# Performance work log

Measured on AMD Instinct MI355X. Metric: run time of the kernel, lower is better.

Reference implementation:

```python
import jax, jax.numpy as jnp
import numpy as np

EPS = 1e-3          # module eps
LAPLACE_EPS = 1e-5  # LaplaceModel eps
N_TAPS = 5
N_DELAY = 1
N_ITER = 5


def _mag_sq(x):
    return x.real ** 2 + x.imag ** 2


def _laplace_weights(Y):
    # LaplaceModel: r = 1 / clamp(2*sqrt(sum_f |Y|^2), eps), broadcast over freq
    denom = 2.0 * jnp.sqrt(jnp.sum(_mag_sq(Y), axis=-2, keepdims=True))
    w = 1.0 / jnp.maximum(denom, LAPLACE_EPS)
    return jnp.broadcast_to(w, Y.shape)


def _make_xbar(X):
    # X_bar[..., c, f, t, n] = X[..., c, f, n - (N_TAPS + N_DELAY) + t], zero-padded
    pad = N_TAPS + N_DELAY
    n_frames = X.shape[-1]
    pad_cfg = [(0, 0)] * (X.ndim - 1) + [(pad, 0)]
    Xp = jnp.pad(X, pad_cfg)
    taps = [Xp[..., t:t + n_frames] for t in range(N_TAPS)]
    return jnp.stack(taps, axis=-2)  # (..., n_chan, n_freq, n_taps, n_frames)


def _demix_derev(X, X_bar, W, H):
    reverb = jnp.einsum('...cfdt,...dftn->...cfn', H, X_bar)
    sep = jnp.einsum('...cfd,...dfn->...cfn', W, X)
    return sep - reverb


def _one_iter(Y, X_bar, W, H):
    n_src = Y.shape[-3]
    n_chan = X_bar.shape[-4]
    n_frames = Y.shape[-1]
    weights = _laplace_weights(Y)
    # rescaling step
    g = jnp.maximum(jnp.mean(_mag_sq(Y), axis=(-2, -1), keepdims=True), EPS)
    gs = jnp.sqrt(g)
    Y = Y / jnp.maximum(gs, EPS)
    W = W / jnp.maximum(gs, EPS)
    H = H / jnp.maximum(gs[..., None], EPS)
    weights = weights * g
    # ISS source updates (type 1)
    inv_nf = 1.0 / n_frames
    for src in range(n_src):
        Ys = Y[..., src, :, :]
        v_num = jnp.einsum('...cfn,...cfn,...fn->...cf', weights, Y, Ys.conj()) * inv_nf
        v_den = jnp.einsum('...cfn,...fn->...cf', weights, _mag_sq(Ys)) * inv_nf
        v = v_num / jnp.maximum(v_den, EPS)
        v_s = 1.0 - 1.0 / jnp.sqrt(jnp.maximum(v_den[..., src, :], EPS))
        v = v.at[..., src, :].set(v_s.astype(v.dtype))
        Y = Y - v[..., None] * Ys[..., None, :, :]
        W = W - jnp.einsum('...cf,...fd->...cfd', v, W[..., src, :, :])
        H = H - jnp.einsum('...cf,...fdt->...cfdt', v, H[..., src, :, :, :])
    # ISS tap updates (type 3)
    for src in range(n_chan):
        for tap in range(N_TAPS):
            Xst = X_bar[..., src, :, tap, :]
            v_num = jnp.einsum('...cfn,...cfn,...fn->...cf', weights, Y, Xst.conj())
            v_den = jnp.einsum('...cfn,...fn->...cf', weights, _mag_sq(Xst))
            v = v_num / jnp.maximum(v_den, EPS)
            Y = Y - v[..., None] * Xst[..., None, :, :]
            H = H.at[..., src, tap].add(v)
    return Y, W, H


def _forward(X):
    batch_shape = X.shape[:-3]
    n_chan, n_freq, n_frames = X.shape[-3:]
    n_src = n_chan  # determined case (n_src=None)
    X_bar = _make_xbar(X)
    eye = jnp.maximum(jnp.eye(n_src, n_chan, dtype=X.real.dtype), EPS)
    W = jnp.broadcast_to(eye[:, None, :].astype(X.dtype), batch_shape + (n_src, n_freq, n_chan))
    H = jnp.zeros(batch_shape + (n_src, n_freq, n_chan, N_TAPS), dtype=X.dtype)
    Y = _demix_derev(X, X_bar, W, H)
    for _ in range(N_ITER):
        Y, W, H = _one_iter(Y, X_bar, W, H)
    return jnp.stack([Y.real, Y.imag], axis=0)


def setup_inputs() -> dict:
    key = jax.random.key(0)
    k1, k2 = jax.random.split(key)
    shape = (2, 4, 512, 1000)  # (batch, n_chan, n_freq, n_frames)
    X_real = jax.random.normal(k1, shape, dtype=jnp.float32)
    X_imag = jax.random.normal(k2, shape, dtype=jnp.float32)
    return {"X_real": X_real, "X_imag": X_imag}


def reference(X_real, X_imag):
    X = jax.lax.complex(X_real, X_imag)
    return _forward(X)
```

## Files before the change

### kernel.cpp

```cpp
#include <hip/hip_runtime.h>


constexpr int NCH = 4;
constexpr int NFQ = 512;
constexpr int NFR = 1000;
constexpr int NIT = 5;
constexpr float EPSV  = 1e-3f;
constexpr float INVNF = 1.0f / 1000.0f;
constexpr float INVFN = 1.0f / (512.0f * 1000.0f);
constexpr size_t PLANE = 4096000;
constexpr size_t CSTRIDE = (size_t)NFQ * NFR;

__device__ __forceinline__ float fast_rcp(float x) { return __builtin_amdgcn_rcpf(x); }
__device__ __forceinline__ float fast_rsq(float x) { return __builtin_amdgcn_rsqf(x); }

template <int CTRL>
__device__ __forceinline__ float dpp_add(float x) {
  return x + __int_as_float(__builtin_amdgcn_update_dpp(
      0, __float_as_int(x), CTRL, 0xF, 0xF, true));
}
__device__ __forceinline__ float wave_red(float x) {
  x = dpp_add<0xB1>(x);
  x = dpp_add<0x4E>(x);
  x = dpp_add<0x141>(x);
  x = dpp_add<0x140>(x);
  x = dpp_add<0x142>(x);
  x = dpp_add<0x143>(x);
  return __int_as_float(__builtin_amdgcn_readlane(__float_as_int(x), 63));
}

__global__ __launch_bounds__(256, 4)
void init_y(const float* __restrict__ Xr, const float* __restrict__ Xi,
            float* __restrict__ Y, float* __restrict__ mag)
{
  const int bf = blockIdx.x, b = bf >> 9, f = bf & 511;
  const size_t base = ((size_t)b * NCH * NFQ + f) * NFR;
  const int tid = threadIdx.x;
  if (tid < 250) {
    const int nq = 4 * tid;
    float4 xr[4], xi[4];
    #pragma unroll
    for (int c = 0; c < 4; ++c) {
      xr[c] = *(const float4*)(Xr + base + (size_t)c * CSTRIDE + nq);
      xi[c] = *(const float4*)(Xi + base + (size_t)c * CSTRIDE + nq);
    }
    float4 sr, si;
    sr.x = xr[0].x+xr[1].x+xr[2].x+xr[3].x;  si.x = xi[0].x+xi[1].x+xi[2].x+xi[3].x;
    sr.y = xr[0].y+xr[1].y+xr[2].y+xr[3].y;  si.y = xi[0].y+xi[1].y+xi[2].y+xi[3].y;
    sr.z = xr[0].z+xr[1].z+xr[2].z+xr[3].z;  si.z = xi[0].z+xi[1].z+xi[2].z+xi[3].z;
    sr.w = xr[0].w+xr[1].w+xr[2].w+xr[3].w;  si.w = xi[0].w+xi[1].w+xi[2].w+xi[3].w;
    #pragma unroll
    for (int c = 0; c < 4; ++c) {
      float4 yr, yi;
      yr.x = 0.999f*xr[c].x + 0.001f*sr.x;  yi.x = 0.999f*xi[c].x + 0.001f*si.x;
      yr.y = 0.999f*xr[c].y + 0.001f*sr.y;  yi.y = 0.999f*xi[c].y + 0.001f*si.y;
      yr.z = 0.999f*xr[c].z + 0.001f*sr.z;  yi.z = 0.999f*xi[c].z + 0.001f*si.z;
      yr.w = 0.999f*xr[c].w + 0.001f*sr.w;  yi.w = 0.999f*xi[c].w + 0.001f*si.w;
      *(float4*)(Y + base + (size_t)c * CSTRIDE + nq)         = yr;
      *(float4*)(Y + base + (size_t)c * CSTRIDE + nq + PLANE) = yi;
      if (mag) {
        float4 m;
        m.x = yr.x*yr.x + yi.x*yi.x;  m.y = yr.y*yr.y + yi.y*yi.y;
        m.z = yr.z*yr.z + yi.z*yi.z;  m.w = yr.w*yr.w + yi.w*yi.w;
        *(float4*)(mag + base + (size_t)c * CSTRIDE + nq) = m;
      }
    }
  }
}

__global__ __launch_bounds__(256, 4)
void partial_mag(const float* __restrict__ mag, float* __restrict__ part2)
{
  const int id = blockIdx.x;
  const int k = id & 15, c = (id >> 4) & 3, b = id >> 6;
  const int tid = threadIdx.x;
  if (tid < 250) {
    const int nq = 4 * tid;
    const float* base = mag + ((size_t)((b*4+c)*NFQ + k*32)) * NFR + nq;
    float4 acc = make_float4(0.f, 0.f, 0.f, 0.f);
    for (int ff = 0; ff < 32; ++ff) {
      const float4 v = *(const float4*)(base + (size_t)ff * NFR);
      acc.x += v.x; acc.y += v.y; acc.z += v.z; acc.w += v.w;
    }
    *(float4*)(part2 + ((size_t)((b*4+c)*16 + k)) * NFR + nq) = acc;
  }
}

__global__ __launch_bounds__(256, 4)
void finish_mag(const float* __restrict__ part2, float* __restrict__ sumf)
{
  const int t = blockIdx.x * 256 + threadIdx.x;
  if (t < 2000) {
    const int b = t / 1000, r = t - 1000 * b;
    const int c = r / 250,  qn = r - 250 * c;
    const float* base = part2 + ((size_t)((b*4+c)*16)) * NFR + 4*qn;
    float4 acc = make_float4(0.f, 0.f, 0.f, 0.f);
    #pragma unroll
    for (int k = 0; k < 16; ++k) {
      const float4 v = *(const float4*)(base + (size_t)k * NFR);
      acc.x += v.x; acc.y += v.y; acc.z += v.z; acc.w += v.w;
    }
    *(float4*)(sumf + (size_t)b*4000 + c*1000 + 4*qn) = acc;
  }
}

__global__ __launch_bounds__(256, 4)
void partial_sumf(const float* __restrict__ Y, float* __restrict__ part)
{
  const int id = blockIdx.x;
  const int q = id & 31, c = (id >> 5) & 3, b = id >> 7;
  const size_t base = (size_t)(b * NCH + c) * CSTRIDE + (size_t)q * 16 * NFR;
  float acc[4] = {0.f, 0.f, 0.f, 0.f};
  for (int ff = 0; ff < 16; ++ff) {
    #pragma unroll
    for (int k = 0; k < 4; ++k) {
      const int n = threadIdx.x + 256 * k;
      if (n < NFR) {
        const float r = Y[base + (size_t)ff * NFR + n];
        const float i = Y[base + (size_t)ff * NFR + n + PLANE];
        acc[k] = fmaf(r, r, acc[k]);
        acc[k] = fmaf(i, i, acc[k]);
      }
    }
  }
  #pragma unroll
  for (int k = 0; k < 4; ++k) {
    const int n = threadIdx.x + 256 * k;
    if (n < NFR) part[((size_t)(b * NCH + c) * 32 + q) * NFR + n] = acc[k];
  }
}
__global__ __launch_bounds__(256, 4)
void finish_sumf(const float* __restrict__ part, float* __restrict__ sumf)
{
  const int o = blockIdx.x * 256 + threadIdx.x;
  if (o < 8000) {
    const int b = o / 4000;
    const int rem = o - b * 4000;
    const int c = rem / 1000;
    const int n = rem - c * 1000;
    const float* p = part + ((size_t)(b * NCH + c) * 32) * NFR + n;
    float s = 0.f;
    for (int q = 0; q < 32; ++q) s += p[(size_t)q * NFR];
    sumf[o] = s;
  }
}

__global__ __launch_bounds__(128, 2)
void iter_c(const float* __restrict__ Xr, const float* __restrict__ Xi,
            float* __restrict__ Y, const float* __restrict__ sumf,
            float* __restrict__ mag)
{
  __shared__ float xre[NCH][NFR];
  __shared__ float xim[NCH][NFR];
  __shared__ float red[2][2][12];
  __shared__ float gred[2][4];

  const int tid  = threadIdx.x;
  const int lane = tid & 63;
  const int wid  = tid >> 6;
  const int ow   = wid ^ 1;
  const int bf   = blockIdx.x, b = bf >> 9, f = bf & 511;
  const size_t base = ((size_t)b * NCH * NFQ + f) * NFR;
  const int nb = 512 * wid + lane;

  for (int j = tid; j < NCH * 250; j += 128) {
    const int c = j / 250, q = j - c * 250;
    *(float4*)(&xre[c][4*q]) = *(const float4*)(Xr + base + (size_t)c*CSTRIDE + 4*q);
    *(float4*)(&xim[c][4*q]) = *(const float4*)(Xi + base + (size_t)c*CSTRIDE + 4*q);
  }

  float w[8][4], invgs[4];
  {
    float sfr[8][4];
    const float* sfb = sumf + b * 4000;
    #pragma unroll
    for (int s = 0; s < 8; ++s) {
      const int na = min(nb + 64*s, 999);
      #pragma unroll
      for (int c = 0; c < 4; ++c) sfr[s][c] = sfb[c*1000 + na];
    }
    float gp[4] = {0.f, 0.f, 0.f, 0.f};
    #pragma unroll
    for (int s = 0; s < 8; ++s) {
      const bool valid = (nb + 64*s) < NFR;
      #pragma unroll
      for (int c = 0; c < 4; ++c) gp[c] += valid ? sfr[s][c] : 0.f;
    }
    #pragma unroll
    for (int c = 0; c < 4; ++c) gp[c] = wave_red(gp[c]);
    if (lane == 0) {
      #pragma unroll
      for (int c = 0; c < 4; ++c) gred[wid][c] = gp[c];
    }
    __syncthreads();

    #pragma unroll
    for (int c = 0; c < 4; ++c) {
      const float g = fmaxf((gred[0][c] + gred[1][c]) * INVFN, EPSV);
      invgs[c] = fast_rsq(g);
      #pragma unroll
      for (int s = 0; s < 8; ++s) {
        const bool valid = (nb + 64*s) < NFR;
        w[s][c] = valid ? g * fminf(0.5f * fast_rsq(sfr[s][c]), 1e5f) : 0.f;
      }
    }
  }

  float yre[8][4], yim[8][4];
  #pragma unroll
  for (int s = 0; s < 8; ++s) {
    const int na = min(nb + 64*s, 999);
    #pragma unroll
    for (int c = 0; c < 4; ++c) {
      yre[s][c] = Y[base + (size_t)c*CSTRIDE + na] * invgs[c];
      yim[s][c] = Y[base + (size_t)c*CSTRIDE + na + PLANE] * invgs[c];
    }
  }

  int par = 0;
  float p[12], vr_[4], vi_[4];

  #pragma unroll
  for (int src = 0; src < 4; ++src) {
    #pragma unroll
    for (int j = 0; j < 12; ++j) p[j] = 0.f;
    #pragma unroll
    for (int s = 0; s < 8; ++s) {
      const float zr = yre[s][src], zi = yim[s][src];
      const float zz = zr*zr + zi*zi;
      #pragma unroll
      for (int c = 0; c < 4; ++c) {
        const float wk = w[s][c];
        p[8+c] = fmaf(wk, zz, p[8+c]);
        if (c != src) {
          p[c]   = fmaf(wk, yre[s][c]*zr + yim[s][c]*zi, p[c]);
          p[4+c] = fmaf(wk, yim[s][c]*zr - yre[s][c]*zi, p[4+c]);
        }
      }
    }
    #pragma unroll
    for (int j = 0; j < 12; ++j)
      if (j != src && j != 4 + src) p[j] = wave_red(p[j]);
    if (lane == 0) {
      #pragma unroll
      for (int j = 0; j < 12; ++j) red[par][wid][j] = p[j];
    }
    __syncthreads();
    #pragma unroll
    for (int j = 0; j < 12; ++j) p[j] += red[par][ow][j];
    par ^= 1;

    float vd[4];
    #pragma unroll
    for (int c = 0; c < 4; ++c) vd[c] = fmaxf(p[8+c] * INVNF, EPSV);
    #pragma unroll
    for (int c = 0; c < 4; ++c) {
      const float inv = INVNF * fast_rcp(vd[c]);
      vr_[c] = p[c] * inv;  vi_[c] = p[4+c] * inv;
    }
    vr_[src] = 1.0f - fast_rsq(vd[src]);  vi_[src] = 0.0f;

    #pragma unroll
    for (int s = 0; s < 8; ++s) {
      const float zr = yre[s][src], zi = yim[s][src];
      #pragma unroll
      for (int c = 0; c < 4; ++c) {
        yre[s][c] -= vr_[c]*zr - vi_[c]*zi;
        yim[s][c] -= vr_[c]*zi + vi_[c]*zr;
      }
    }
  }

  for (int src = 0; src < 4; ++src) {
    const float* px = xre[src];
    const float* py = xim[src];
    float xwr[8][5], xwi[8][5];
    #pragma unroll
    for (int s = 0; s < 8; ++s) {
      #pragma unroll
      for (int o = 0; o < 5; ++o) {
        const int m = nb + 64*s - 6 + o;
        int mc = m;
        if (s == 0) mc = max(m, 0);
        if (s == 7) mc = min(m, 999);
        float vr = px[mc], vi = py[mc];
        if (s == 0) {
          vr = (m >= 0) ? vr : 0.f;
          vi = (m >= 0) ? vi : 0.f;
        }
        xwr[s][o] = vr; xwi[s][o] = vi;
      }
    }

    #pragma unroll
    for (int tap = 0; tap < 5; ++tap) {
      #pragma unroll
      for (int j = 0; j < 12; ++j) p[j] = 0.f;
      #pragma unroll
      for (int s = 0; s < 8; ++s) {
        const float zr = xwr[s][tap], zi = xwi[s][tap];
        const float zz = zr*zr + zi*zi;
        #pragma unroll
        for (int c = 0; c < 4; ++c) {
          const float wk = w[s][c];
          p[8+c] = fmaf(wk, zz, p[8+c]);
          p[c]   = fmaf(wk, yre[s][c]*zr + yim[s][c]*zi, p[c]);
          p[4+c] = fmaf(wk, yim[s][c]*zr - yre[s][c]*zi, p[4+c]);
        }
      }
      #pragma unroll
      for (int j = 0; j < 12; ++j) p[j] = wave_red(p[j]);
      if (lane == 0) {
        #pragma unroll
        for (int j = 0; j < 12; ++j) red[par][wid][j] = p[j];
      }
      __syncthreads();
      #pragma unroll
      for (int j = 0; j < 12; ++j) p[j] += red[par][ow][j];
      par ^= 1;

      #pragma unroll
      for (int c = 0; c < 4; ++c) {
        const float inv = fast_rcp(fmaxf(p[8+c], EPSV));
        vr_[c] = p[c] * inv;  vi_[c] = p[4+c] * inv;
      }
      #pragma unroll
      for (int s = 0; s < 8; ++s) {
        const float zr = xwr[s][tap], zi = xwi[s][tap];
        #pragma unroll
        for (int c = 0; c < 4; ++c) {
          yre[s][c] -= vr_[c]*zr - vi_[c]*zi;
          yim[s][c] -= vr_[c]*zi + vi_[c]*zr;
        }
      }
    }
  }

  #pragma unroll
  for (int s = 0; s < 8; ++s) {
    const int n = nb + 64*s;
    if (n < NFR) {
      #pragma unroll
      for (int c = 0; c < 4; ++c) {
        const float yr = yre[s][c], yi = yim[s][c];
        Y[base + (size_t)c*CSTRIDE + n]         = yr;
        Y[base + (size_t)c*CSTRIDE + n + PLANE] = yi;
        if (mag) mag[base + (size_t)c*CSTRIDE + n] = yr*yr + yi*yi;
      }
    }
  }
}

extern "C" void kernel_launch(void* const* d_in, const int* in_sizes, int n_in,
                              void* d_out, int out_size, void* d_ws, size_t ws_size,
                              hipStream_t stream)
{
  const float* Xr = (const float*)d_in[0];
  const float* Xi = (const float*)d_in[1];
  float* Y = (float*)d_out;

  const bool big_ws = ws_size >= (size_t)(4096000 + 128000 + 8000) * 4;
  if (big_ws) {
    float* mag   = (float*)d_ws;
    float* part2 = mag + 4096000;
    float* sumf  = part2 + 128000;
    init_y<<<1024, 256, 0, stream>>>(Xr, Xi, Y, mag);
    for (int it = 0; it < NIT; ++it) {
      partial_mag<<<128, 256, 0, stream>>>(mag, part2);
      finish_mag<<<8, 256, 0, stream>>>(part2, sumf);
      iter_c<<<1024, 128, 0, stream>>>(Xr, Xi, Y, sumf,
                                       (it < NIT - 1) ? mag : nullptr);
    }
  } else {
    float* part = (float*)d_ws;
    float* sumf = part + 256000;
    init_y<<<1024, 256, 0, stream>>>(Xr, Xi, Y, nullptr);
    for (int it = 0; it < NIT; ++it) {
      partial_sumf<<<256, 256, 0, stream>>>(Y, part);
      finish_sumf<<<32, 256, 0, stream>>>(part, sumf);
      iter_c<<<1024, 128, 0, stream>>>(Xr, Xi, Y, sumf, nullptr);
    }
  }
}
```

Measured before the change: 369.1 us.

## Split each frequency row across four waves instead of two in iter_c

The per-(batch,freq) ISS kernel now runs 256 threads (four waves) per block, each thread holding 4 frame slots instead of 8. The cross-wave reduction becomes a four-way sum of float4-packed partials in shared memory. The aim is to cut per-thread register pressure and serial work, raising occupancy and latency hiding. The cost is more wave reductions and a wider barrier for each of the 24 sequential ISS steps.

```diff
diff --git a/kernel.cpp b/kernel.cpp
--- a/kernel.cpp
+++ b/kernel.cpp
@@ -27,6 +27,9 @@
   x = dpp_add<0x142>(x);
   x = dpp_add<0x143>(x);
   return __int_as_float(__builtin_amdgcn_readlane(__float_as_int(x), 63));
+}
+__device__ __forceinline__ float4 f4add(float4 a, float4 b) {
+  return make_float4(a.x + b.x, a.y + b.y, a.z + b.z, a.w + b.w);
 }
 
 __global__ __launch_bounds__(256, 4)
@@ -145,70 +148,69 @@
   }
 }
 
-__global__ __launch_bounds__(128, 2)
+__global__ __launch_bounds__(256, 4)
 void iter_c(const float* __restrict__ Xr, const float* __restrict__ Xi,
             float* __restrict__ Y, const float* __restrict__ sumf,
             float* __restrict__ mag)
 {
-  __shared__ float xre[NCH][NFR];
-  __shared__ float xim[NCH][NFR];
-  __shared__ float red[2][2][12];
-  __shared__ float gred[2][4];
+  __shared__ float  xre[NCH][NFR];
+  __shared__ float  xim[NCH][NFR];
+  __shared__ float4 redv[2][4][3];
+  __shared__ float4 gredv[4];
 
   const int tid  = threadIdx.x;
   const int lane = tid & 63;
   const int wid  = tid >> 6;
-  const int ow   = wid ^ 1;
   const int bf   = blockIdx.x, b = bf >> 9, f = bf & 511;
   const size_t base = ((size_t)b * NCH * NFQ + f) * NFR;
-  const int nb = 512 * wid + lane;
-
-  for (int j = tid; j < NCH * 250; j += 128) {
+  const int nb = 256 * wid + lane;
+
+  for (int j = tid; j < NCH * 250; j += 256) {
     const int c = j / 250, q = j - c * 250;
     *(float4*)(&xre[c][4*q]) = *(const float4*)(Xr + base + (size_t)c*CSTRIDE + 4*q);
     *(float4*)(&xim[c][4*q]) = *(const float4*)(Xi + base + (size_t)c*CSTRIDE + 4*q);
   }
 
-  float w[8][4], invgs[4];
+  float w[4][4], invgs[4];
   {
-    float sfr[8][4];
+    float sfr[4][4];
     const float* sfb = sumf + b * 4000;
     #pragma unroll
-    for (int s = 0; s < 8; ++s) {
+    for (int s = 0; s < 4; ++s) {
       const int na = min(nb + 64*s, 999);
       #pragma unroll
       for (int c = 0; c < 4; ++c) sfr[s][c] = sfb[c*1000 + na];
     }
     float gp[4] = {0.f, 0.f, 0.f, 0.f};
     #pragma unroll
-    for (int s = 0; s < 8; ++s) {
+    for (int s = 0; s < 4; ++s) {
       const bool valid = (nb + 64*s) < NFR;
       #pragma unroll
       for (int c = 0; c < 4; ++c) gp[c] += valid ? sfr[s][c] : 0.f;
     }
     #pragma unroll
     for (int c = 0; c < 4; ++c) gp[c] = wave_red(gp[c]);
-    if (lane == 0) {
-      #pragma unroll
-      for (int c = 0; c < 4; ++c) gred[wid][c] = gp[c];
-    }
+    if (lane == 0) gredv[wid] = make_float4(gp[0], gp[1], gp[2], gp[3]);
     __syncthreads();
 
+    const float4 gv = f4add(f4add(gredv[0], gredv[1]), f4add(gredv[2], gredv[3]));
+    float g[4];
+    g[0] = fmaxf(gv.x * INVFN, EPSV);  g[1] = fmaxf(gv.y * INVFN, EPSV);
+    g[2] = fmaxf(gv.z * INVFN, EPSV);  g[3] = fmaxf(gv.w * INVFN, EPSV);
     #pragma unroll
     for (int c = 0; c < 4; ++c) {
-      const float g = fmaxf((gred[0][c] + gred[1][c]) * INVFN, EPSV);
-      invgs[c] = fast_rsq(g);
-      #pragma unroll
-      for (int s = 0; s < 8; ++s) {
+      invgs[c] = fast_rsq(g[c]);
+      #pragma unroll
+      for (int s = 0; s < 4; ++s) {
         const bool valid = (nb + 64*s) < NFR;
-        w[s][c] = valid ? g * fminf(0.5f * fast_rsq(sfr[s][c]), 1e5f) : 0.f;
-      }
-    }
-  }
-
-  float yre[8][4], yim[8][4];
+        w[s][c] = valid ? g[c] * fminf(0.5f * fast_rsq(sfr[s][c]), 1e5f) : 0.f;
+      }
+    }
+  }
+
+  float yre[4][4], yim[4][4];
   #pragma unroll
-  for (int s = 0; s < 8; ++s) {
+  for (int s = 0; s < 4; ++s) {
     const int na = min(nb + 64*s, 999);
     #pragma unroll
     for (int c = 0; c < 4; ++c) {
@@ -225,7 +227,7 @@
     #pragma unroll
     for (int j = 0; j < 12; ++j) p[j] = 0.f;
     #pragma unroll
-    for (int s = 0; s < 8; ++s) {
+    for (int s = 0; s < 4; ++s) {
       const float zr = yre[s][src], zi = yim[s][src];
       const float zz = zr*zr + zi*zi;
       #pragma unroll
@@ -242,12 +244,22 @@
     for (int j = 0; j < 12; ++j)
       if (j != src && j != 4 + src) p[j] = wave_red(p[j]);
     if (lane == 0) {
-      #pragma unroll
-      for (int j = 0; j < 12; ++j) red[par][wid][j] = p[j];
+      redv[par][wid][0] = make_float4(p[0], p[1], p[2],  p[3]);
+      redv[par][wid][1] = make_float4(p[4], p[5], p[6],  p[7]);
+      redv[par][wid][2] = make_float4(p[8], p[9], p[10], p[11]);
     }
     __syncthreads();
-    #pragma unroll
-    for (int j = 0; j < 12; ++j) p[j] += red[par][ow][j];
+    {
+      const float4 s0 = f4add(f4add(redv[par][0][0], redv[par][1][0]),
+                              f4add(redv[par][2][0], redv[par][3][0]));
+      const float4 s1 = f4add(f4add(redv[par][0][1], redv[par][1][1]),
+                              f4add(redv[par][2][1], redv[par][3][1]));
+      const float4 s2 = f4add(f4add(redv[par][0][2], redv[par][1][2]),
+                              f4add(redv[par][2][2], redv[par][3][2]));
+      p[0]=s0.x; p[1]=s0.y; p[2]=s0.z;  p[3]=s0.w;
+      p[4]=s1.x; p[5]=s1.y; p[6]=s1.z;  p[7]=s1.w;
+      p[8]=s2.x; p[9]=s2.y; p[10]=s2.z; p[11]=s2.w;
+    }
     par ^= 1;
 
     float vd[4];
@@ -261,7 +273,7 @@
     vr_[src] = 1.0f - fast_rsq(vd[src]);  vi_[src] = 0.0f;
 
     #pragma unroll
-    for (int s = 0; s < 8; ++s) {
+    for (int s = 0; s < 4; ++s) {
       const float zr = yre[s][src], zi = yim[s][src];
       #pragma unroll
       for (int c = 0; c < 4; ++c) {
@@ -274,15 +286,15 @@
   for (int src = 0; src < 4; ++src) {
     const float* px = xre[src];
     const float* py = xim[src];
-    float xwr[8][5], xwi[8][5];
-    #pragma unroll
-    for (int s = 0; s < 8; ++s) {
+    float xwr[4][5], xwi[4][5];
+    #pragma unroll
+    for (int s = 0; s < 4; ++s) {
       #pragma unroll
       for (int o = 0; o < 5; ++o) {
         const int m = nb + 64*s - 6 + o;
         int mc = m;
         if (s == 0) mc = max(m, 0);
-        if (s == 7) mc = min(m, 999);
+        if (s == 3) mc = min(m, 999);
         float vr = px[mc], vi = py[mc];
         if (s == 0) {
           vr = (m >= 0) ? vr : 0.f;
@@ -297,7 +309,7 @@
       #pragma unroll
       for (int j = 0; j < 12; ++j) p[j] = 0.f;
       #pragma unroll
-      for (int s = 0; s < 8; ++s) {
+      for (int s = 0; s < 4; ++s) {
         const float zr = xwr[s][tap], zi = xwi[s][tap];
         const float zz = zr*zr + zi*zi;
         #pragma unroll
@@ -311,12 +323,22 @@
       #pragma unroll
       for (int j = 0; j < 12; ++j) p[j] = wave_red(p[j]);
       if (lane == 0) {
-        #pragma unroll
-        for (int j = 0; j < 12; ++j) red[par][wid][j] = p[j];
+        redv[par][wid][0] = make_float4(p[0], p[1], p[2],  p[3]);
+        redv[par][wid][1] = make_float4(p[4], p[5], p[6],  p[7]);
+        redv[par][wid][2] = make_float4(p[8], p[9], p[10], p[11]);
       }
       __syncthreads();
-      #pragma unroll
-      for (int j = 0; j < 12; ++j) p[j] += red[par][ow][j];
+      {
+        const float4 s0 = f4add(f4add(redv[par][0][0], redv[par][1][0]),
+                                f4add(redv[par][2][0], redv[par][3][0]));
+        const float4 s1 = f4add(f4add(redv[par][0][1], redv[par][1][1]),
+                                f4add(redv[par][2][1], redv[par][3][1]));
+        const float4 s2 = f4add(f4add(redv[par][0][2], redv[par][1][2]),
+                                f4add(redv[par][2][2], redv[par][3][2]));
+        p[0]=s0.x; p[1]=s0.y; p[2]=s0.z;  p[3]=s0.w;
+        p[4]=s1.x; p[5]=s1.y; p[6]=s1.z;  p[7]=s1.w;
+        p[8]=s2.x; p[9]=s2.y; p[10]=s2.z; p[11]=s2.w;
+      }
       par ^= 1;
 
       #pragma unroll
@@ -325,7 +347,7 @@
         vr_[c] = p[c] * inv;  vi_[c] = p[4+c] * inv;
       }
       #pragma unroll
-      for (int s = 0; s < 8; ++s) {
+      for (int s = 0; s < 4; ++s) {
         const float zr = xwr[s][tap], zi = xwi[s][tap];
         #pragma unroll
         for (int c = 0; c < 4; ++c) {
@@ -337,7 +359,7 @@
   }
 
   #pragma unroll
-  for (int s = 0; s < 8; ++s) {
+  for (int s = 0; s < 4; ++s) {
     const int n = nb + 64*s;
     if (n < NFR) {
       #pragma unroll
@@ -368,7 +390,7 @@
     for (int it = 0; it < NIT; ++it) {
       partial_mag<<<128, 256, 0, stream>>>(mag, part2);
       finish_mag<<<8, 256, 0, stream>>>(part2, sumf);
-      iter_c<<<1024, 128, 0, stream>>>(Xr, Xi, Y, sumf,
+      iter_c<<<1024, 256, 0, stream>>>(Xr, Xi, Y, sumf,
                                        (it < NIT - 1) ? mag : nullptr);
     }
   } else {
@@ -378,7 +400,7 @@
     for (int it = 0; it < NIT; ++it) {
       partial_sumf<<<256, 256, 0, stream>>>(Y, part);
       finish_sumf<<<32, 256, 0, stream>>>(part, sumf);
-      iter_c<<<1024, 128, 0, stream>>>(Xr, Xi, Y, sumf, nullptr);
-    }
-  }
-}
+      iter_c<<<1024, 256, 0, stream>>>(Xr, Xi, Y, sumf, nullptr);
+    }
+  }
+}
```

New measurement: 450.2 us. +22.0%, slower.
